# Performance work log

Measured on AMD Instinct MI355X. Metric: run time of the kernel, lower is better.

The kernel has to match this reference:

```python
import math
import jax, jax.numpy as jnp
import numpy as np

HIDDEN = 1024
HEADS = 16
HEAD_DIM = HIDDEN // HEADS  # 64
SEQ = 4096
PATCH = 4064  # num rotated (patch) tokens; last PATCH positions get RoPE
EPS = 1e-6


def setup_inputs() -> dict:
    key = jax.random.key(0)
    ks = jax.random.split(key, 8)
    return {
        "x": jax.random.normal(ks[0], (1, SEQ, HIDDEN), dtype=jnp.float32),
        "rope_cos": jax.random.uniform(ks[1], (PATCH, HEAD_DIM // 2), dtype=jnp.float32),
        "rope_sin": jax.random.uniform(ks[2], (PATCH, HEAD_DIM // 2), dtype=jnp.float32),
        "wq": jax.random.normal(ks[3], (HIDDEN, HIDDEN), dtype=jnp.float32) / math.sqrt(HIDDEN),
        "wk": jax.random.normal(ks[4], (HIDDEN, HIDDEN), dtype=jnp.float32) / math.sqrt(HIDDEN),
        "wv": jax.random.normal(ks[5], (HIDDEN, HIDDEN), dtype=jnp.float32) / math.sqrt(HIDDEN),
        "wo": jax.random.normal(ks[6], (HIDDEN, HIDDEN), dtype=jnp.float32) / math.sqrt(HIDDEN),
        "q_norm_w": jnp.ones((HEAD_DIM,), dtype=jnp.float32),
        "k_norm_w": jnp.ones((HEAD_DIM,), dtype=jnp.float32),
    }


def _rms_norm(t, w):
    # RMSNorm over the last (head_dim) axis
    return t * jax.lax.rsqrt(jnp.mean(t * t, axis=-1, keepdims=True) + EPS) * w


def _apply_rope(t, cos, sin):
    # t: [b, s, h, d]; rotate only the last PATCH positions, pairwise complex mul
    b, s, h, d = t.shape
    P = cos.shape[0]
    tail = t[:, s - P:].reshape(b, P, h, d // 2, 2)
    x0, x1 = tail[..., 0], tail[..., 1]
    c = cos[None, :, None, :]
    sn = sin[None, :, None, :]
    rot = jnp.stack([x0 * c - x1 * sn, x0 * sn + x1 * c], axis=-1).reshape(b, P, h, d)
    return jnp.concatenate([t[:, : s - P], rot], axis=1)


def reference(x, rope_cos, rope_sin, wq, wk, wv, wo, q_norm_w, k_norm_w):
    b, s, _ = x.shape
    q = (x @ wq.T).reshape(b, s, HEADS, HEAD_DIM)
    k = (x @ wk.T).reshape(b, s, HEADS, HEAD_DIM)
    v = (x @ wv.T).reshape(b, s, HEADS, HEAD_DIM)
    q = _rms_norm(q, q_norm_w)
    k = _rms_norm(k, k_norm_w)
    q = _apply_rope(q, rope_cos, rope_sin)
    k = _apply_rope(k, rope_cos, rope_sin)
    q = q / math.sqrt(HEAD_DIM)
    scores = jnp.einsum('bqhd,bkhd->bhqk', q, k)
    attn = jax.nn.softmax(scores.astype(jnp.float32), axis=-1)
    out = jnp.einsum('bhqk,bkhd->bqhd', attn, v).reshape(b, s, HIDDEN)
    return out @ wo.T
```

## Files before the change

### kernel.cpp

```cpp
#include <hip/hip_runtime.h>
#include <hip/hip_bf16.h>
#include <stdint.h>

#define HIDDEN 1024
#define HEADS 16
#define HEAD_DIM 64
#define SEQ 4096
#define PATCH 4064
#define SKIP 32

typedef __attribute__((ext_vector_type(8))) short bf16x8;
typedef __attribute__((ext_vector_type(4))) float f32x4;
typedef __attribute__((ext_vector_type(2))) float f32x2;
typedef __attribute__((ext_vector_type(16))) float f32x16;

__device__ __forceinline__ float b2f(unsigned short u){
  union{uint32_t i; float f;} c; c.i = ((uint32_t)u)<<16; return c.f;
}
__device__ __forceinline__ unsigned short f2b(float f){
  union{float f; uint32_t i;} c; c.f=f;
  uint32_t r = c.i + 0x7fffu + ((c.i>>16)&1u);
  return (unsigned short)(r>>16);
}
__device__ __forceinline__ uint32_t cvtpk(float a, float b){
  uint32_t r;
  asm("v_cvt_pk_bf16_f32 %0, %1, %2" : "=v"(r) : "v"(a), "v"(b));
  return r;
}

#define GLD16(gp, lp) __builtin_amdgcn_global_load_lds( \
    (const __attribute__((address_space(1))) void*)(gp), \
    (__attribute__((address_space(3))) void*)(lp), 16, 0, 0)

__global__ __launch_bounds__(256) void convert_all(
    const float* __restrict__ x,  const float* __restrict__ wq,
    const float* __restrict__ wk, const float* __restrict__ wv,
    const float* __restrict__ wo,
    unsigned short* __restrict__ xb,  unsigned short* __restrict__ wqb,
    unsigned short* __restrict__ wkb, unsigned short* __restrict__ wvb,
    unsigned short* __restrict__ wob)
{
  size_t u = (size_t)blockIdx.x*256 + threadIdx.x;
  size_t e = u*8;
  const float* src; unsigned short* dst; size_t off;
  if      (e < 4194304ull) { src=x;  dst=xb;  off=e;            }
  else if (e < 5242880ull) { src=wq; dst=wqb; off=e-4194304ull; }
  else if (e < 6291456ull) { src=wk; dst=wkb; off=e-5242880ull; }
  else if (e < 7340032ull) { src=wv; dst=wvb; off=e-6291456ull; }
  else                     { src=wo; dst=wob; off=e-7340032ull; }
  float4 v0 = *(const float4*)(src+off);
  float4 v1 = *(const float4*)(src+off+4);
  union { bf16x8 v; unsigned short h[8]; } o;
  o.h[0]=f2b(v0.x); o.h[1]=f2b(v0.y); o.h[2]=f2b(v0.z); o.h[3]=f2b(v0.w);
  o.h[4]=f2b(v1.x); o.h[5]=f2b(v1.y); o.h[6]=f2b(v1.z); o.h[7]=f2b(v1.w);
  *(bf16x8*)(dst+off) = o.v;
}

template<int MODE>
__global__ __launch_bounds__(256) void gemm_bt(
    const unsigned short* __restrict__ A,
    const unsigned short* __restrict__ B0,
    const unsigned short* __restrict__ B1,
    const unsigned short* __restrict__ B2,
    float* __restrict__ Cf,
    unsigned short* __restrict__ qout, unsigned short* __restrict__ kout,
    unsigned short* __restrict__ vout,
    const float* __restrict__ rc, const float* __restrict__ rs,
    const float* __restrict__ qw, const float* __restrict__ kw,
    int M, int Nper, int K)
{
  __shared__ unsigned short As[128*32];
  __shared__ unsigned short Bs[128*32];
  const int tid = threadIdx.x;
  const int w = tid>>6, l = tid&63;
  const int wm = w>>1, wn = w&1;
  const int g = l>>4, lr = l&15;
  const int bm = blockIdx.x;
  int bn = blockIdx.y;
  const int tilesPer = Nper >> 7;
  const int sel = bn / tilesPer;
  bn -= sel*tilesPer;
  const unsigned short* Bsel = (sel==0) ? B0 : ((sel==1) ? B1 : B2);

  const int off0 = w*1024 + l*16;
  const int r0 = off0>>6, c0 = (off0&63)>>1;
  const int off1 = off0 + 4096;
  const int r1 = off1>>6, c1 = (off1&63)>>1;

  const unsigned short* Ab = A    + (size_t)(bm*128)*K;
  const unsigned short* Bb = Bsel + (size_t)(bn*128)*K;

  f32x4 zero = {0.f,0.f,0.f,0.f};
  f32x4 acc[4][4];
  #pragma unroll
  for (int m=0;m<4;m++)
    #pragma unroll
    for (int n=0;n<4;n++) acc[m][n]=zero;

  for (int kt = 0; kt < K; kt += 32) {
    GLD16(Ab + (size_t)r0*K + kt + c0, (char*)As + off0);
    GLD16(Ab + (size_t)r1*K + kt + c1, (char*)As + off1);
    GLD16(Bb + (size_t)r0*K + kt + c0, (char*)Bs + off0);
    GLD16(Bb + (size_t)r1*K + kt + c1, (char*)Bs + off1);
    __syncthreads();
    bf16x8 a[4], b[4];
    #pragma unroll
    for (int m=0;m<4;m++)
      a[m] = *(const bf16x8*)&As[(wm*64 + m*16 + lr)*32 + g*8];
    #pragma unroll
    for (int n=0;n<4;n++)
      b[n] = *(const bf16x8*)&Bs[(wn*64 + n*16 + lr)*32 + g*8];
    #pragma unroll
    for (int m=0;m<4;m++)
      #pragma unroll
      for (int n=0;n<4;n++)
        acc[m][n] = __builtin_amdgcn_mfma_f32_16x16x32_bf16(a[m], b[n], acc[m][n], 0,0,0);
    __syncthreads();
  }

  if constexpr (MODE == 0) {
    #pragma unroll
    for (int m=0;m<4;m++){
      const int row = bm*128 + wm*64 + m*16 + g*4;
      #pragma unroll
      for (int n=0;n<4;n++){
        const int col = bn*128 + wn*64 + n*16 + lr;
        #pragma unroll
        for (int r=0;r<4;r++)
          Cf[(size_t)(row+r)*Nper + col] = acc[m][n][r];
      }
    }
  } else {
    if (sel <= 1) {
      const float* nw = (sel==0) ? qw : kw;
      unsigned short* dst = (sel==0) ? qout : kout;
      const float scl = (sel==0) ? 0.18033688011112042f : 1.0f;
      float wl[4];
      #pragma unroll
      for (int n=0;n<4;n++) wl[n] = nw[n*16+lr];
      const int hglob = bn*2 + wn;
      #pragma unroll
      for (int m=0;m<4;m++){
        const int rowb = bm*128 + wm*64 + m*16 + g*4;
        float rn[4];
        #pragma unroll
        for (int r=0;r<4;r++){
          float ss = 0.f;
          #pragma unroll
          for (int n=0;n<4;n++) ss += acc[m][n][r]*acc[m][n][r];
          ss += __shfl_xor(ss,1); ss += __shfl_xor(ss,2);
          ss += __shfl_xor(ss,4); ss += __shfl_xor(ss,8);
          rn[r] = rsqrtf(ss*(1.f/64.f) + 1e-6f);
        }
        #pragma unroll
        for (int r=0;r<4;r++){
          const int row = rowb + r;
          const int p = row - SKIP;
          #pragma unroll
          for (int n=0;n<4;n++){
            float v = acc[m][n][r]*rn[r]*wl[n];
            float c = 1.f, sn = 0.f;
            if (p >= 0){
              const int d2 = (n*16+lr)>>1;
              c  = rc[p*(HEAD_DIM/2) + d2];
              sn = rs[p*(HEAD_DIM/2) + d2];
            }
            const float partner = __shfl_xor(v, 1);
            const float o2 = (lr&1) ? (partner*sn + v*c) : (v*c - partner*sn);
            dst[(size_t)row*HIDDEN + hglob*64 + n*16 + lr] = f2b(o2*scl);
          }
        }
      }
    } else {
      #pragma unroll
      for (int m=0;m<4;m++){
        const int row = bm*128 + wm*64 + m*16 + g*4;
        #pragma unroll
        for (int n=0;n<4;n++){
          const int col = bn*128 + wn*64 + n*16 + lr;
          #pragma unroll
          for (int r=0;r<4;r++)
            vout[(size_t)(row+r)*HIDDEN + col] = f2b(acc[m][n][r]);
        }
      }
    }
  }
}

__global__ __launch_bounds__(256) void transpose_v(
    const unsigned short* __restrict__ v, unsigned short* __restrict__ vt)
{
  __shared__ unsigned short t[64*72];
  const int h = blockIdx.y;
  const int s0 = blockIdx.x * 64;
  const int tid = threadIdx.x;
  #pragma unroll
  for (int i=0;i<2;i++){
    const int e = tid + i*256;
    const int r = e>>3, cc = (e&7)*8;
    *(bf16x8*)&t[r*72+cc] = *(const bf16x8*)(v + (size_t)(s0+r)*HIDDEN + h*HEAD_DIM + cc);
  }
  __syncthreads();
  #pragma unroll
  for (int i=0;i<2;i++){
    const int e = tid + i*256;
    const int d = e>>3, sc = (e&7)*8;
    union { bf16x8 v8; unsigned short h8[8]; } o;
    #pragma unroll
    for (int j=0;j<8;j++){
      const int x  = sc + j;
      const int px = (x & ~12) | ((x&4)<<1) | ((x&8)>>1);
      o.h8[j] = t[px*72 + d];
    }
    *(bf16x8*)(vt + (size_t)(h*HEAD_DIM + d)*SEQ + s0 + sc) = o.v8;
  }
}

__device__ __forceinline__ void softmax_pack(f32x16 (&st)[2], f32x2 &lacc, bf16x8 (&pf)[4]){
  float pv[32];
  #pragma unroll
  for (int i=0;i<16;i++){
    pv[i]    = __builtin_amdgcn_exp2f(st[0][i]);
    pv[16+i] = __builtin_amdgcn_exp2f(st[1][i]);
  }
  #pragma unroll
  for (int i=0;i<8;i++){
    f32x2 a; a.x = pv[2*i];    a.y = pv[2*i+1];    lacc += a;
    f32x2 b; b.x = pv[16+2*i]; b.y = pv[16+2*i+1]; lacc += b;
  }
  #pragma unroll
  for (int t2=0; t2<2; t2++)
    #pragma unroll
    for (int e=0; e<2; e++){
      union { uint32_t u4[4]; bf16x8 v8; } pu;
      #pragma unroll
      for (int u=0; u<4; u++)
        pu.u4[u] = cvtpk(pv[t2*16+e*8+2*u], pv[t2*16+e*8+2*u+1]);
      pf[2*t2+e] = pu.v8;
    }
}

__global__ __launch_bounds__(256, 2) void attn_kernel(
    const unsigned short* __restrict__ q, const unsigned short* __restrict__ k,
    const unsigned short* __restrict__ vt, unsigned short* __restrict__ po,
    float* __restrict__ lbuf)
{
  __shared__ unsigned short smem[16384];
  const int fid = blockIdx.x + 16*(blockIdx.y + 16*blockIdx.z);
  const int h    = (fid&7)*2 + ((fid>>3)&1);
  const int rem  = fid>>4;
  const int q0   = (rem&15)*256;
  const int half = rem>>4;
  const int tid = threadIdx.x;
  const int w = tid>>6, l = tid&63;
  const int hi = l>>5, lo = l&31;
  const int NT = SEQ/64/2;
  const int tbase = half * NT;

  const int cA = tid, cB = tid + 256;
  const int rA = cA>>3, rB = cB>>3;
  const int colA = ((cA&7)*16) ^ ((rA&7)<<4);
  const int colB = ((cB&7)*16) ^ ((rB&7)<<4);
  const unsigned short* kA = k  + (size_t)rA*HIDDEN + h*HEAD_DIM + (colA>>1);
  const unsigned short* kB = k  + (size_t)rB*HIDDEN + h*HEAD_DIM + (colB>>1);
  const unsigned short* vA = vt + ((size_t)(h*HEAD_DIM + rA))*SEQ + (colA>>1);
  const unsigned short* vB = vt + ((size_t)(h*HEAD_DIM + rB))*SEQ + (colB>>1);

#define STAGE(b, kOffE, vOffE) do { \
    GLD16(kA + (kOffE), (char*)smem + (b)*16384 + cA*16); \
    GLD16(kB + (kOffE), (char*)smem + (b)*16384 + cB*16); \
    GLD16(vA + (vOffE), (char*)smem + (b)*16384 + 8192 + cA*16); \
    GLD16(vB + (vOffE), (char*)smem + (b)*16384 + 8192 + cB*16); \
  } while(0)

  const int swz = (lo&7)<<4;
  int colo[4];
  #pragma unroll
  for (int ks=0; ks<4; ks++) colo[ks] = ((2*ks+hi)*16) ^ swz;

  bf16x8 qf0[4], qf1[4];
  {
    const unsigned short* qp = q + (size_t)(q0 + w*64 + lo)*HIDDEN + h*HEAD_DIM;
    #pragma unroll
    for (int ks=0; ks<4; ks++){
      qf0[ks] = *(const bf16x8*)(qp + ks*16 + hi*8);
      qf1[ks] = *(const bf16x8*)(qp + 32*HIDDEN + ks*16 + hi*8);
    }
  }

  f32x16 ot0[2], ot1[2];
  #pragma unroll
  for (int m2=0;m2<2;m2++)
    #pragma unroll
    for (int i=0;i<16;i++){ ot0[m2][i] = 0.f; ot1[m2][i] = 0.f; }
  f32x2 lacc0 = {0.f,0.f}, lacc1 = {0.f,0.f};

  STAGE(0, (size_t)tbase*64*HIDDEN, (size_t)tbase*64);

  for (int t = 0; t < NT; ++t) {
    const int buf = t & 1;
    __syncthreads();
    if (t+1 < NT) {
      const size_t ta = (size_t)(tbase + t + 1);
      STAGE((t+1)&1, ta*64*HIDDEN, ta*64);
    }

    const char* Kb = (const char*)smem + buf*16384;
    const char* Vb = Kb + 8192;

    f32x16 st0[2], st1[2];
    __builtin_amdgcn_s_setprio(1);
    #pragma unroll
    for (int c=0;c<2;c++){
      #pragma unroll
      for (int i=0;i<16;i++){ st0[c][i] = 0.f; st1[c][i] = 0.f; }
      #pragma unroll
      for (int ks=0; ks<4; ks++){
        bf16x8 a = *(const bf16x8*)(Kb + (32*c+lo)*128 + colo[ks]);
        st0[c] = __builtin_amdgcn_mfma_f32_32x32x16_bf16(a, qf0[ks], st0[c], 0,0,0);
        st1[c] = __builtin_amdgcn_mfma_f32_32x32x16_bf16(a, qf1[ks], st1[c], 0,0,0);
      }
    }
    __builtin_amdgcn_s_setprio(0);

    bf16x8 pf0[4], pf1[4];
    softmax_pack(st0, lacc0, pf0);
    softmax_pack(st1, lacc1, pf1);

    __builtin_amdgcn_s_setprio(1);
    #pragma unroll
    for (int m2=0;m2<2;m2++)
      #pragma unroll
      for (int ks=0; ks<4; ks++){
        bf16x8 a = *(const bf16x8*)(Vb + (32*m2+lo)*128 + colo[ks]);
        ot0[m2] = __builtin_amdgcn_mfma_f32_32x32x16_bf16(a, pf0[ks], ot0[m2], 0,0,0);
        ot1[m2] = __builtin_amdgcn_mfma_f32_32x32x16_bf16(a, pf1[ks], ot1[m2], 0,0,0);
      }
    __builtin_amdgcn_s_setprio(0);
  }

  {
    float ls0 = lacc0.x + lacc0.y;
    ls0 += __shfl_xor(ls0, 32);
    float ls1 = lacc1.x + lacc1.y;
    ls1 += __shfl_xor(ls1, 32);
    if (hi == 0){
      lbuf[(size_t)half*HEADS*SEQ + h*SEQ + q0 + w*64 + lo]      = ls0;
      lbuf[(size_t)half*HEADS*SEQ + h*SEQ + q0 + w*64 + 32 + lo] = ls1;
    }
  }

  __syncthreads();
  #pragma unroll
  for (int m2=0;m2<2;m2++)
    #pragma unroll
    for (int f=0; f<4; f++)
      #pragma unroll
      for (int u=0; u<2; u++){
        const int d = 32*m2 + 8*f + 4*hi + 2*u;
        const uint32_t w0 = cvtpk(ot0[m2][4*f+2*u], ot0[m2][4*f+2*u+1]);
        *(uint32_t*)((char*)smem + (w*64+lo)*128 + ((d*2) ^ swz)) = w0;
        const uint32_t w1 = cvtpk(ot1[m2][4*f+2*u], ot1[m2][4*f+2*u+1]);
        *(uint32_t*)((char*)smem + (w*64+32+lo)*128 + ((d*2) ^ swz)) = w1;
      }
  __syncthreads();
  unsigned short* pout = po + (size_t)half*SEQ*HIDDEN;
  #pragma unroll
  for (int rr=0; rr<2; rr++){
    const int ql = rr*128 + (tid>>1), xh = tid&1;
    #pragma unroll
    for (int i=0;i<4;i++){
      const int cb = xh*64 + i*16;
      bf16x8 vv = *(const bf16x8*)((const char*)smem + ql*128 + (cb ^ ((ql&7)<<4)));
      *(bf16x8*)(pout + (size_t)(q0+ql)*HIDDEN + h*HEAD_DIM + (cb>>1)) = vv;
    }
  }
#undef STAGE
}

__global__ __launch_bounds__(256) void combine_halves(
    const unsigned short* __restrict__ po, const float* __restrict__ lbuf,
    unsigned short* __restrict__ at)
{
  const size_t e = ((size_t)blockIdx.x*256 + threadIdx.x)*8;
  const int qrow = (int)(e >> 10);
  const int h = (int)((e >> 6) & 15);
  const float li = 1.0f / (lbuf[h*SEQ + qrow] + lbuf[HEADS*SEQ + h*SEQ + qrow]);
  union { bf16x8 v; unsigned short s[8]; } a, b, o;
  a.v = *(const bf16x8*)(po + e);
  b.v = *(const bf16x8*)(po + (size_t)SEQ*HIDDEN + e);
  #pragma unroll
  for (int j=0;j<8;j++)
    o.s[j] = f2b((b2f(a.s[j]) + b2f(b.s[j])) * li);
  *(bf16x8*)(at + e) = o.v;
}

extern "C" void kernel_launch(void* const* d_in, const int* in_sizes, int n_in,
                              void* d_out, int out_size, void* d_ws, size_t ws_size,
                              hipStream_t stream)
{
  const float* x  = (const float*)d_in[0];
  const float* rc = (const float*)d_in[1];
  const float* rs = (const float*)d_in[2];
  const float* wq = (const float*)d_in[3];
  const float* wk = (const float*)d_in[4];
  const float* wv = (const float*)d_in[5];
  const float* wo = (const float*)d_in[6];
  const float* qw = (const float*)d_in[7];
  const float* kw = (const float*)d_in[8];
  float* out = (float*)d_out;

  char* ws = (char*)d_ws;
  const size_t MB = 1024*1024;
  unsigned short* xb  = (unsigned short*)(ws + 0);
  unsigned short* wqb = (unsigned short*)(ws + 8*MB);
  unsigned short* wkb = (unsigned short*)(ws + 10*MB);
  unsigned short* wvb = (unsigned short*)(ws + 12*MB);
  unsigned short* wob = (unsigned short*)(ws + 14*MB);
  unsigned short* qkv = (unsigned short*)(ws + 16*MB);
  unsigned short* qb = qkv;
  unsigned short* kb = qkv + (size_t)SEQ*HIDDEN;
  unsigned short* vb = qkv + (size_t)2*SEQ*HIDDEN;
  unsigned short* vt = (unsigned short*)(ws + 0);
  float*          lbuf = (float*)(ws + 8*MB);
  unsigned short* po = (unsigned short*)(ws + 32*MB);
  unsigned short* at = (unsigned short*)(ws + 40*MB);

  convert_all<<<4096, 256, 0, stream>>>(x, wq, wk, wv, wo, xb, wqb, wkb, wvb, wob);
  gemm_bt<1><<<dim3(32,24), 256, 0, stream>>>(
      xb, wqb, wkb, wvb, nullptr, qb, kb, vb, rc, rs, qw, kw,
      SEQ, HIDDEN, HIDDEN);
  transpose_v<<<dim3(64,16), 256, 0, stream>>>(vb, vt);
  attn_kernel<<<dim3(16,16,2), 256, 0, stream>>>(qb, kb, vt, po, lbuf);
  combine_halves<<<2048, 256, 0, stream>>>(po, lbuf, at);
  gemm_bt<0><<<dim3(32,8), 256, 0, stream>>>(
      at, wob, wob, wob, out, nullptr, nullptr, nullptr, nullptr, nullptr, nullptr, nullptr,
      SEQ, HIDDEN, HIDDEN);
}
```

Baseline: 181.4 us.

## Rewrite QKV projection GEMM with 256x256 tiles, double-buffered LDS and swizzle

The fused QKV projection moves to a dedicated kernel using 512-thread blocks, 256x256 output tiles, double-buffered LDS staging with an XOR swizzle, and interleaved loads and MFMAs under setprio. The aim is to hide global-load latency and LDS bank conflicts and to raise arithmetic intensity compared with the old 128x128 single-buffered loop that synchronised twice per k-step. In exchange it launches only 192 blocks, fewer than the CU count, and uses more registers, which may limit occupancy. The output GEMM is split into its own simpler kernel with unchanged behaviour.

```diff
diff --git a/kernel.cpp b/kernel.cpp
--- a/kernel.cpp
+++ b/kernel.cpp
@@ -56,18 +56,153 @@
   *(bf16x8*)(dst+off) = o.v;
 }
 
-template<int MODE>
-__global__ __launch_bounds__(256) void gemm_bt(
+__global__ __launch_bounds__(512, 2) void gemm_qkv(
     const unsigned short* __restrict__ A,
     const unsigned short* __restrict__ B0,
     const unsigned short* __restrict__ B1,
     const unsigned short* __restrict__ B2,
-    float* __restrict__ Cf,
     unsigned short* __restrict__ qout, unsigned short* __restrict__ kout,
     unsigned short* __restrict__ vout,
     const float* __restrict__ rc, const float* __restrict__ rs,
-    const float* __restrict__ qw, const float* __restrict__ kw,
-    int M, int Nper, int K)
+    const float* __restrict__ qw, const float* __restrict__ kw)
+{
+  __shared__ unsigned short smem[32768];
+  const int tid = threadIdx.x;
+  const int wid = tid>>6, l = tid&63;
+  const int wm = wid>>2, wn = wid&3;
+  const int g = l>>4, lr = l&15;
+  const int bm = blockIdx.x;
+  const int bn = blockIdx.y;
+  const int sel = bn>>2, hb = bn&3;
+  const unsigned short* Bsel = (sel==0) ? B0 : ((sel==1) ? B1 : B2);
+
+  const int strow = tid>>2;
+  const int skey = ((((tid>>2)&3) ^ ((tid>>4)&3))<<4);
+  const int scol = ((tid&3)*16) ^ skey;
+  const unsigned short* pA0 = A    + (size_t)(bm*256 + strow)*1024 + (scol>>1);
+  const unsigned short* pA1 = pA0 + (size_t)128*1024;
+  const unsigned short* pB0 = Bsel + (size_t)(hb*256 + strow)*1024 + (scol>>1);
+  const unsigned short* pB1 = pB0 + (size_t)128*1024;
+  const int dA0 = tid*16, dA1 = tid*16 + 8192;
+  const int dB0 = 16384 + tid*16, dB1 = 24576 + tid*16;
+
+#define STAGEQ(db, ktE) do { \
+    GLD16(pA0 + (ktE), (char*)smem + (db) + dA0); \
+    GLD16(pA1 + (ktE), (char*)smem + (db) + dA1); \
+    GLD16(pB0 + (ktE), (char*)smem + (db) + dB0); \
+    GLD16(pB1 + (ktE), (char*)smem + (db) + dB1); } while(0)
+
+  const int rkey = (((lr&3) ^ ((lr>>2)&3))<<4);
+  const int rcol = (g*16) ^ rkey;
+  const int aBase = (wm*128 + lr)*64 + rcol;
+  const int bBase = 16384 + (wn*64 + lr)*64 + rcol;
+
+  f32x4 acc[8][4];
+  #pragma unroll
+  for (int m=0;m<8;m++)
+    #pragma unroll
+    for (int n=0;n<4;n++) acc[m][n] = (f32x4){0.f,0.f,0.f,0.f};
+
+  STAGEQ(0, 0);
+  asm volatile("s_waitcnt vmcnt(0)" ::: "memory");
+  __builtin_amdgcn_s_barrier();
+  __builtin_amdgcn_sched_barrier(0);
+
+  for (int t = 0; t < 32; ++t) {
+    const int db  = (t&1)<<15;
+    const int ndb = db ^ 32768;
+    bf16x8 af[4], bf[4];
+    #pragma unroll
+    for (int i=0;i<4;i++) af[i] = *(const bf16x8*)((char*)smem + db + aBase + i*1024);
+    #pragma unroll
+    for (int i=0;i<4;i++) bf[i] = *(const bf16x8*)((char*)smem + db + bBase + i*1024);
+    if (t+1 < 32) STAGEQ(ndb, (t+1)*32);
+    __builtin_amdgcn_s_barrier();
+    __builtin_amdgcn_s_setprio(1);
+    #pragma unroll
+    for (int m=0;m<4;m++)
+      #pragma unroll
+      for (int n=0;n<4;n++)
+        acc[m][n] = __builtin_amdgcn_mfma_f32_16x16x32_bf16(af[m], bf[n], acc[m][n], 0,0,0);
+    __builtin_amdgcn_s_setprio(0);
+    __builtin_amdgcn_s_barrier();
+    #pragma unroll
+    for (int i=0;i<4;i++) af[i] = *(const bf16x8*)((char*)smem + db + aBase + 4096 + i*1024);
+    #pragma unroll
+    for (int i=0;i<4;i++) bf[i] = *(const bf16x8*)((char*)smem + db + bBase + i*1024);
+    asm volatile("s_waitcnt vmcnt(0)" ::: "memory");
+    __builtin_amdgcn_s_barrier();
+    __builtin_amdgcn_sched_barrier(0);
+    __builtin_amdgcn_s_setprio(1);
+    #pragma unroll
+    for (int m=0;m<4;m++)
+      #pragma unroll
+      for (int n=0;n<4;n++)
+        acc[4+m][n] = __builtin_amdgcn_mfma_f32_16x16x32_bf16(af[m], bf[n], acc[4+m][n], 0,0,0);
+    __builtin_amdgcn_s_setprio(0);
+    __builtin_amdgcn_s_barrier();
+  }
+
+  if (sel <= 1) {
+    const float* nw = (sel==0) ? qw : kw;
+    unsigned short* dst = (sel==0) ? qout : kout;
+    const float scl = (sel==0) ? 0.18033688011112042f : 1.0f;
+    float wl[4];
+    #pragma unroll
+    for (int n=0;n<4;n++) wl[n] = nw[n*16+lr];
+    const int hglob = hb*4 + wn;
+    #pragma unroll
+    for (int mf=0; mf<8; mf++){
+      const int rowb = bm*256 + wm*128 + mf*16 + g*4;
+      float rn4[4];
+      #pragma unroll
+      for (int r=0;r<4;r++){
+        float ss = 0.f;
+        #pragma unroll
+        for (int n=0;n<4;n++) ss += acc[mf][n][r]*acc[mf][n][r];
+        ss += __shfl_xor(ss,1); ss += __shfl_xor(ss,2);
+        ss += __shfl_xor(ss,4); ss += __shfl_xor(ss,8);
+        rn4[r] = rsqrtf(ss*(1.f/64.f) + 1e-6f);
+      }
+      #pragma unroll
+      for (int r=0;r<4;r++){
+        const int row = rowb + r;
+        const int p = row - SKIP;
+        #pragma unroll
+        for (int n=0;n<4;n++){
+          float v = acc[mf][n][r]*rn4[r]*wl[n];
+          float c = 1.f, sn = 0.f;
+          if (p >= 0){
+            const int d2 = (n*16+lr)>>1;
+            c  = rc[p*(HEAD_DIM/2) + d2];
+            sn = rs[p*(HEAD_DIM/2) + d2];
+          }
+          const float partner = __shfl_xor(v, 1);
+          const float o2 = (lr&1) ? (partner*sn + v*c) : (v*c - partner*sn);
+          dst[(size_t)row*HIDDEN + hglob*64 + n*16 + lr] = f2b(o2*scl);
+        }
+      }
+    }
+  } else {
+    #pragma unroll
+    for (int mf=0; mf<8; mf++){
+      const int rowb = bm*256 + wm*128 + mf*16 + g*4;
+      #pragma unroll
+      for (int n=0;n<4;n++){
+        const int col = hb*256 + wn*64 + n*16 + lr;
+        #pragma unroll
+        for (int r=0;r<4;r++)
+          vout[(size_t)(rowb+r)*HIDDEN + col] = f2b(acc[mf][n][r]);
+      }
+    }
+  }
+#undef STAGEQ
+}
+
+__global__ __launch_bounds__(256) void gemm_out(
+    const unsigned short* __restrict__ A,
+    const unsigned short* __restrict__ B,
+    float* __restrict__ Cf, int M, int N, int K)
 {
   __shared__ unsigned short As[128*32];
   __shared__ unsigned short Bs[128*32];
@@ -76,19 +211,15 @@
   const int wm = w>>1, wn = w&1;
   const int g = l>>4, lr = l&15;
   const int bm = blockIdx.x;
-  int bn = blockIdx.y;
-  const int tilesPer = Nper >> 7;
-  const int sel = bn / tilesPer;
-  bn -= sel*tilesPer;
-  const unsigned short* Bsel = (sel==0) ? B0 : ((sel==1) ? B1 : B2);
+  const int bn = blockIdx.y;
 
   const int off0 = w*1024 + l*16;
   const int r0 = off0>>6, c0 = (off0&63)>>1;
   const int off1 = off0 + 4096;
   const int r1 = off1>>6, c1 = (off1&63)>>1;
 
-  const unsigned short* Ab = A    + (size_t)(bm*128)*K;
-  const unsigned short* Bb = Bsel + (size_t)(bn*128)*K;
+  const unsigned short* Ab = A + (size_t)(bm*128)*K;
+  const unsigned short* Bb = B + (size_t)(bn*128)*K;
 
   f32x4 zero = {0.f,0.f,0.f,0.f};
   f32x4 acc[4][4];
@@ -117,72 +248,15 @@
         acc[m][n] = __builtin_amdgcn_mfma_f32_16x16x32_bf16(a[m], b[n], acc[m][n], 0,0,0);
     __syncthreads();
   }
-
-  if constexpr (MODE == 0) {
-    #pragma unroll
-    for (int m=0;m<4;m++){
-      const int row = bm*128 + wm*64 + m*16 + g*4;
-      #pragma unroll
-      for (int n=0;n<4;n++){
-        const int col = bn*128 + wn*64 + n*16 + lr;
-        #pragma unroll
-        for (int r=0;r<4;r++)
-          Cf[(size_t)(row+r)*Nper + col] = acc[m][n][r];
-      }
-    }
-  } else {
-    if (sel <= 1) {
-      const float* nw = (sel==0) ? qw : kw;
-      unsigned short* dst = (sel==0) ? qout : kout;
-      const float scl = (sel==0) ? 0.18033688011112042f : 1.0f;
-      float wl[4];
-      #pragma unroll
-      for (int n=0;n<4;n++) wl[n] = nw[n*16+lr];
-      const int hglob = bn*2 + wn;
-      #pragma unroll
-      for (int m=0;m<4;m++){
-        const int rowb = bm*128 + wm*64 + m*16 + g*4;
-        float rn[4];
-        #pragma unroll
-        for (int r=0;r<4;r++){
-          float ss = 0.f;
-          #pragma unroll
-          for (int n=0;n<4;n++) ss += acc[m][n][r]*acc[m][n][r];
-          ss += __shfl_xor(ss,1); ss += __shfl_xor(ss,2);
-          ss += __shfl_xor(ss,4); ss += __shfl_xor(ss,8);
-          rn[r] = rsqrtf(ss*(1.f/64.f) + 1e-6f);
-        }
-        #pragma unroll
-        for (int r=0;r<4;r++){
-          const int row = rowb + r;
-          const int p = row - SKIP;
-          #pragma unroll
-          for (int n=0;n<4;n++){
-            float v = acc[m][n][r]*rn[r]*wl[n];
-            float c = 1.f, sn = 0.f;
-            if (p >= 0){
-              const int d2 = (n*16+lr)>>1;
-              c  = rc[p*(HEAD_DIM/2) + d2];
-              sn = rs[p*(HEAD_DIM/2) + d2];
-            }
-            const float partner = __shfl_xor(v, 1);
-            const float o2 = (lr&1) ? (partner*sn + v*c) : (v*c - partner*sn);
-            dst[(size_t)row*HIDDEN + hglob*64 + n*16 + lr] = f2b(o2*scl);
-          }
-        }
-      }
-    } else {
-      #pragma unroll
-      for (int m=0;m<4;m++){
-        const int row = bm*128 + wm*64 + m*16 + g*4;
-        #pragma unroll
-        for (int n=0;n<4;n++){
-          const int col = bn*128 + wn*64 + n*16 + lr;
-          #pragma unroll
-          for (int r=0;r<4;r++)
-            vout[(size_t)(row+r)*HIDDEN + col] = f2b(acc[m][n][r]);
-        }
-      }
+  #pragma unroll
+  for (int m=0;m<4;m++){
+    const int row = bm*128 + wm*64 + m*16 + g*4;
+    #pragma unroll
+    for (int n=0;n<4;n++){
+      const int col = bn*128 + wn*64 + n*16 + lr;
+      #pragma unroll
+      for (int r=0;r<4;r++)
+        Cf[(size_t)(row+r)*N + col] = acc[m][n][r];
     }
   }
 }
@@ -427,13 +501,10 @@
   unsigned short* at = (unsigned short*)(ws + 40*MB);
 
   convert_all<<<4096, 256, 0, stream>>>(x, wq, wk, wv, wo, xb, wqb, wkb, wvb, wob);
-  gemm_bt<1><<<dim3(32,24), 256, 0, stream>>>(
-      xb, wqb, wkb, wvb, nullptr, qb, kb, vb, rc, rs, qw, kw,
-      SEQ, HIDDEN, HIDDEN);
+  gemm_qkv<<<dim3(16,12), 512, 0, stream>>>(
+      xb, wqb, wkb, wvb, qb, kb, vb, rc, rs, qw, kw);
   transpose_v<<<dim3(64,16), 256, 0, stream>>>(vb, vt);
   attn_kernel<<<dim3(16,16,2), 256, 0, stream>>>(qb, kb, vt, po, lbuf);
   combine_halves<<<2048, 256, 0, stream>>>(po, lbuf, at);
-  gemm_bt<0><<<dim3(32,8), 256, 0, stream>>>(
-      at, wob, wob, wob, out, nullptr, nullptr, nullptr, nullptr, nullptr, nullptr, nullptr,
-      SEQ, HIDDEN, HIDDEN);
-}
+  gemm_out<<<dim3(32,8), 256, 0, stream>>>(at, wob, out, SEQ, HIDDEN, HIDDEN);
+}
```

New measurement: 181.7 us. No clear change (+0.2%).

## Double-buffer GEMM LDS tiles and widen attention KV tiles to 128

Applied to the files above, without the earlier changes.

The projection GEMM now uses two LDS stages: the next K-slice is loaded while MFMAs run on the current one, and only one barrier per iteration remains. The attention kernel loads 128 keys per stage instead of 64 and processes them as two 64-key sub-blocks, which halves the number of barriers and stage loads. In exchange, attention LDS grows to 64KB per block, which may limit how many blocks fit per CU alongside launch_bounds(256,2).

```diff
diff --git a/kernel.cpp b/kernel.cpp
--- a/kernel.cpp
+++ b/kernel.cpp
@@ -69,8 +69,7 @@
     const float* __restrict__ qw, const float* __restrict__ kw,
     int M, int Nper, int K)
 {
-  __shared__ unsigned short As[128*32];
-  __shared__ unsigned short Bs[128*32];
+  __shared__ unsigned short smem[16384];
   const int tid = threadIdx.x;
   const int w = tid>>6, l = tid&63;
   const int wm = w>>1, wn = w&1;
@@ -90,6 +89,12 @@
   const unsigned short* Ab = A    + (size_t)(bm*128)*K;
   const unsigned short* Bb = Bsel + (size_t)(bn*128)*K;
 
+#define STG(db, kt) do { \
+    GLD16(Ab + (size_t)r0*K + (kt) + c0, (char*)smem + (db) + off0); \
+    GLD16(Ab + (size_t)r1*K + (kt) + c1, (char*)smem + (db) + off1); \
+    GLD16(Bb + (size_t)r0*K + (kt) + c0, (char*)smem + (db) + 8192 + off0); \
+    GLD16(Bb + (size_t)r1*K + (kt) + c1, (char*)smem + (db) + 8192 + off1); } while(0)
+
   f32x4 zero = {0.f,0.f,0.f,0.f};
   f32x4 acc[4][4];
   #pragma unroll
@@ -97,26 +102,26 @@
     #pragma unroll
     for (int n=0;n<4;n++) acc[m][n]=zero;
 
-  for (int kt = 0; kt < K; kt += 32) {
-    GLD16(Ab + (size_t)r0*K + kt + c0, (char*)As + off0);
-    GLD16(Ab + (size_t)r1*K + kt + c1, (char*)As + off1);
-    GLD16(Bb + (size_t)r0*K + kt + c0, (char*)Bs + off0);
-    GLD16(Bb + (size_t)r1*K + kt + c1, (char*)Bs + off1);
+  const int nkt = K >> 5;
+  STG(0, 0);
+  for (int t = 0; t < nkt; ++t) {
     __syncthreads();
+    const int db = (t&1)<<14;
+    if (t+1 < nkt) STG(db^16384, (t+1)*32);
     bf16x8 a[4], b[4];
     #pragma unroll
     for (int m=0;m<4;m++)
-      a[m] = *(const bf16x8*)&As[(wm*64 + m*16 + lr)*32 + g*8];
+      a[m] = *(const bf16x8*)((char*)smem + db + (wm*64 + m*16 + lr)*64 + g*16);
     #pragma unroll
     for (int n=0;n<4;n++)
-      b[n] = *(const bf16x8*)&Bs[(wn*64 + n*16 + lr)*32 + g*8];
+      b[n] = *(const bf16x8*)((char*)smem + db + 8192 + (wn*64 + n*16 + lr)*64 + g*16);
     #pragma unroll
     for (int m=0;m<4;m++)
       #pragma unroll
       for (int n=0;n<4;n++)
         acc[m][n] = __builtin_amdgcn_mfma_f32_16x16x32_bf16(a[m], b[n], acc[m][n], 0,0,0);
-    __syncthreads();
-  }
+  }
+#undef STG
 
   if constexpr (MODE == 0) {
     #pragma unroll
@@ -245,7 +250,7 @@
     const unsigned short* __restrict__ vt, unsigned short* __restrict__ po,
     float* __restrict__ lbuf)
 {
-  __shared__ unsigned short smem[16384];
+  __shared__ unsigned short smem[32768];
   const int fid = blockIdx.x + 16*(blockIdx.y + 16*blockIdx.z);
   const int h    = (fid&7)*2 + ((fid>>3)&1);
   const int rem  = fid>>4;
@@ -254,23 +259,35 @@
   const int tid = threadIdx.x;
   const int w = tid>>6, l = tid&63;
   const int hi = l>>5, lo = l&31;
-  const int NT = SEQ/64/2;
+  const int NT = SEQ/128/2;
   const int tbase = half * NT;
 
-  const int cA = tid, cB = tid + 256;
-  const int rA = cA>>3, rB = cB>>3;
-  const int colA = ((cA&7)*16) ^ ((rA&7)<<4);
-  const int colB = ((cB&7)*16) ^ ((rB&7)<<4);
-  const unsigned short* kA = k  + (size_t)rA*HIDDEN + h*HEAD_DIM + (colA>>1);
-  const unsigned short* kB = k  + (size_t)rB*HIDDEN + h*HEAD_DIM + (colB>>1);
-  const unsigned short* vA = vt + ((size_t)(h*HEAD_DIM + rA))*SEQ + (colA>>1);
-  const unsigned short* vB = vt + ((size_t)(h*HEAD_DIM + rB))*SEQ + (colB>>1);
+  int kcol[4], vcol[4], vrow[4];
+  #pragma unroll
+  for (int i=0;i<4;i++){
+    const int c = tid + i*256;
+    const int rk = c>>3;
+    kcol[i] = ((c&7)*16) ^ ((rk&7)<<4);
+    const int rv = c>>4;
+    vrow[i] = rv;
+    vcol[i] = (((c&7)*16) ^ ((rv&7)<<4)) + ((c>>3)&1)*128;
+  }
+  const unsigned short* kPtr[4]; const unsigned short* vPtr[4];
+  #pragma unroll
+  for (int i=0;i<4;i++){
+    kPtr[i] = k  + (size_t)((tid + i*256)>>3)*HIDDEN + h*HEAD_DIM + (kcol[i]>>1);
+    vPtr[i] = vt + ((size_t)(h*HEAD_DIM + vrow[i]))*SEQ + (vcol[i]>>1);
+  }
 
 #define STAGE(b, kOffE, vOffE) do { \
-    GLD16(kA + (kOffE), (char*)smem + (b)*16384 + cA*16); \
-    GLD16(kB + (kOffE), (char*)smem + (b)*16384 + cB*16); \
-    GLD16(vA + (vOffE), (char*)smem + (b)*16384 + 8192 + cA*16); \
-    GLD16(vB + (vOffE), (char*)smem + (b)*16384 + 8192 + cB*16); \
+    GLD16(kPtr[0] + (kOffE), (char*)smem + (b)*32768 + (tid      )*16); \
+    GLD16(kPtr[1] + (kOffE), (char*)smem + (b)*32768 + (tid+ 256 )*16); \
+    GLD16(kPtr[2] + (kOffE), (char*)smem + (b)*32768 + (tid+ 512 )*16); \
+    GLD16(kPtr[3] + (kOffE), (char*)smem + (b)*32768 + (tid+ 768 )*16); \
+    GLD16(vPtr[0] + (vOffE), (char*)smem + (b)*32768 + 16384 + (tid      )*16); \
+    GLD16(vPtr[1] + (vOffE), (char*)smem + (b)*32768 + 16384 + (tid+ 256 )*16); \
+    GLD16(vPtr[2] + (vOffE), (char*)smem + (b)*32768 + 16384 + (tid+ 512 )*16); \
+    GLD16(vPtr[3] + (vOffE), (char*)smem + (b)*32768 + 16384 + (tid+ 768 )*16); \
   } while(0)
 
   const int swz = (lo&7)<<4;
@@ -295,48 +312,51 @@
     for (int i=0;i<16;i++){ ot0[m2][i] = 0.f; ot1[m2][i] = 0.f; }
   f32x2 lacc0 = {0.f,0.f}, lacc1 = {0.f,0.f};
 
-  STAGE(0, (size_t)tbase*64*HIDDEN, (size_t)tbase*64);
+  STAGE(0, (size_t)tbase*128*HIDDEN, (size_t)tbase*128);
 
   for (int t = 0; t < NT; ++t) {
-    const int buf = t & 1;
     __syncthreads();
     if (t+1 < NT) {
       const size_t ta = (size_t)(tbase + t + 1);
-      STAGE((t+1)&1, ta*64*HIDDEN, ta*64);
-    }
-
-    const char* Kb = (const char*)smem + buf*16384;
-    const char* Vb = Kb + 8192;
-
-    f32x16 st0[2], st1[2];
-    __builtin_amdgcn_s_setprio(1);
-    #pragma unroll
-    for (int c=0;c<2;c++){
-      #pragma unroll
-      for (int i=0;i<16;i++){ st0[c][i] = 0.f; st1[c][i] = 0.f; }
-      #pragma unroll
-      for (int ks=0; ks<4; ks++){
-        bf16x8 a = *(const bf16x8*)(Kb + (32*c+lo)*128 + colo[ks]);
-        st0[c] = __builtin_amdgcn_mfma_f32_32x32x16_bf16(a, qf0[ks], st0[c], 0,0,0);
-        st1[c] = __builtin_amdgcn_mfma_f32_32x32x16_bf16(a, qf1[ks], st1[c], 0,0,0);
+      STAGE((t+1)&1, ta*128*HIDDEN, ta*128);
+    }
+    const char* Kb = (const char*)smem + (t&1)*32768;
+    const char* Vb = Kb + 16384;
+
+    #pragma unroll
+    for (int sub=0; sub<2; ++sub) {
+      const char* Ks = Kb + sub*8192;
+
+      f32x16 st0[2], st1[2];
+      __builtin_amdgcn_s_setprio(1);
+      #pragma unroll
+      for (int c=0;c<2;c++){
+        #pragma unroll
+        for (int i=0;i<16;i++){ st0[c][i] = 0.f; st1[c][i] = 0.f; }
+        #pragma unroll
+        for (int ks=0; ks<4; ks++){
+          bf16x8 a = *(const bf16x8*)(Ks + (32*c+lo)*128 + colo[ks]);
+          st0[c] = __builtin_amdgcn_mfma_f32_32x32x16_bf16(a, qf0[ks], st0[c], 0,0,0);
+          st1[c] = __builtin_amdgcn_mfma_f32_32x32x16_bf16(a, qf1[ks], st1[c], 0,0,0);
+        }
       }
-    }
-    __builtin_amdgcn_s_setprio(0);
-
-    bf16x8 pf0[4], pf1[4];
-    softmax_pack(st0, lacc0, pf0);
-    softmax_pack(st1, lacc1, pf1);
-
-    __builtin_amdgcn_s_setprio(1);
-    #pragma unroll
-    for (int m2=0;m2<2;m2++)
-      #pragma unroll
-      for (int ks=0; ks<4; ks++){
-        bf16x8 a = *(const bf16x8*)(Vb + (32*m2+lo)*128 + colo[ks]);
-        ot0[m2] = __builtin_amdgcn_mfma_f32_32x32x16_bf16(a, pf0[ks], ot0[m2], 0,0,0);
-        ot1[m2] = __builtin_amdgcn_mfma_f32_32x32x16_bf16(a, pf1[ks], ot1[m2], 0,0,0);
-      }
-    __builtin_amdgcn_s_setprio(0);
+      __builtin_amdgcn_s_setprio(0);
+
+      bf16x8 pf0[4], pf1[4];
+      softmax_pack(st0, lacc0, pf0);
+      softmax_pack(st1, lacc1, pf1);
+
+      __builtin_amdgcn_s_setprio(1);
+      #pragma unroll
+      for (int m2=0;m2<2;m2++)
+        #pragma unroll
+        for (int ks=0; ks<4; ks++){
+          bf16x8 a = *(const bf16x8*)(Vb + (32*m2+lo)*256 + sub*128 + colo[ks]);
+          ot0[m2] = __builtin_amdgcn_mfma_f32_32x32x16_bf16(a, pf0[ks], ot0[m2], 0,0,0);
+          ot1[m2] = __builtin_amdgcn_mfma_f32_32x32x16_bf16(a, pf1[ks], ot1[m2], 0,0,0);
+        }
+      __builtin_amdgcn_s_setprio(0);
+    }
   }
 
   {
```

Result: faster. 153.7 us (-15.3%).

## Split attention KV range four ways and double-buffer GEMM shared-memory tiles

Applied to the files above, without the earlier changes.

The attention kernel now splits the key/value sequence into four partitions instead of two. This doubles the grid to 1024 blocks and raises the occupancy hint to 4 blocks per CU, giving more parallel work. The extra partial outputs are placed in spare workspace and in the output buffer, and combine_halves sums four partials and four row-sum arrays. Separately, the bf16 GEMM now double-buffers its A/B tiles in shared memory, prefetching the next K-slice while computing the current one and dropping one barrier per iteration. The cost is more partial-output traffic in the combine step and possible register pressure under the higher occupancy target.

```diff
diff --git a/kernel.cpp b/kernel.cpp
--- a/kernel.cpp
+++ b/kernel.cpp
@@ -69,8 +69,7 @@
     const float* __restrict__ qw, const float* __restrict__ kw,
     int M, int Nper, int K)
 {
-  __shared__ unsigned short As[128*32];
-  __shared__ unsigned short Bs[128*32];
+  __shared__ unsigned short smem[16384];
   const int tid = threadIdx.x;
   const int w = tid>>6, l = tid&63;
   const int wm = w>>1, wn = w&1;
@@ -90,6 +89,12 @@
   const unsigned short* Ab = A    + (size_t)(bm*128)*K;
   const unsigned short* Bb = Bsel + (size_t)(bn*128)*K;
 
+#define STG(db, kt) do { \
+    GLD16(Ab + (size_t)r0*K + (kt) + c0, (char*)smem + (db) + off0); \
+    GLD16(Ab + (size_t)r1*K + (kt) + c1, (char*)smem + (db) + off1); \
+    GLD16(Bb + (size_t)r0*K + (kt) + c0, (char*)smem + (db) + 8192 + off0); \
+    GLD16(Bb + (size_t)r1*K + (kt) + c1, (char*)smem + (db) + 8192 + off1); } while(0)
+
   f32x4 zero = {0.f,0.f,0.f,0.f};
   f32x4 acc[4][4];
   #pragma unroll
@@ -97,26 +102,26 @@
     #pragma unroll
     for (int n=0;n<4;n++) acc[m][n]=zero;
 
-  for (int kt = 0; kt < K; kt += 32) {
-    GLD16(Ab + (size_t)r0*K + kt + c0, (char*)As + off0);
-    GLD16(Ab + (size_t)r1*K + kt + c1, (char*)As + off1);
-    GLD16(Bb + (size_t)r0*K + kt + c0, (char*)Bs + off0);
-    GLD16(Bb + (size_t)r1*K + kt + c1, (char*)Bs + off1);
+  const int nkt = K >> 5;
+  STG(0, 0);
+  for (int t = 0; t < nkt; ++t) {
     __syncthreads();
+    const int db = (t&1)<<14;
+    if (t+1 < nkt) STG(db^16384, (t+1)*32);
     bf16x8 a[4], b[4];
     #pragma unroll
     for (int m=0;m<4;m++)
-      a[m] = *(const bf16x8*)&As[(wm*64 + m*16 + lr)*32 + g*8];
+      a[m] = *(const bf16x8*)((char*)smem + db + (wm*64 + m*16 + lr)*64 + g*16);
     #pragma unroll
     for (int n=0;n<4;n++)
-      b[n] = *(const bf16x8*)&Bs[(wn*64 + n*16 + lr)*32 + g*8];
+      b[n] = *(const bf16x8*)((char*)smem + db + 8192 + (wn*64 + n*16 + lr)*64 + g*16);
     #pragma unroll
     for (int m=0;m<4;m++)
       #pragma unroll
       for (int n=0;n<4;n++)
         acc[m][n] = __builtin_amdgcn_mfma_f32_16x16x32_bf16(a[m], b[n], acc[m][n], 0,0,0);
-    __syncthreads();
-  }
+  }
+#undef STG
 
   if constexpr (MODE == 0) {
     #pragma unroll
@@ -240,9 +245,11 @@
     }
 }
 
-__global__ __launch_bounds__(256, 2) void attn_kernel(
+__global__ __launch_bounds__(256, 4) void attn_kernel(
     const unsigned short* __restrict__ q, const unsigned short* __restrict__ k,
-    const unsigned short* __restrict__ vt, unsigned short* __restrict__ po,
+    const unsigned short* __restrict__ vt,
+    unsigned short* __restrict__ po0, unsigned short* __restrict__ po1,
+    unsigned short* __restrict__ po2, unsigned short* __restrict__ po3,
     float* __restrict__ lbuf)
 {
   __shared__ unsigned short smem[16384];
@@ -254,7 +261,7 @@
   const int tid = threadIdx.x;
   const int w = tid>>6, l = tid&63;
   const int hi = l>>5, lo = l&31;
-  const int NT = SEQ/64/2;
+  const int NT = SEQ/64/4;
   const int tbase = half * NT;
 
   const int cA = tid, cB = tid + 256;
@@ -298,14 +305,12 @@
   STAGE(0, (size_t)tbase*64*HIDDEN, (size_t)tbase*64);
 
   for (int t = 0; t < NT; ++t) {
-    const int buf = t & 1;
     __syncthreads();
     if (t+1 < NT) {
       const size_t ta = (size_t)(tbase + t + 1);
       STAGE((t+1)&1, ta*64*HIDDEN, ta*64);
     }
-
-    const char* Kb = (const char*)smem + buf*16384;
+    const char* Kb = (const char*)smem + (t&1)*16384;
     const char* Vb = Kb + 8192;
 
     f32x16 st0[2], st1[2];
@@ -364,7 +369,7 @@
         *(uint32_t*)((char*)smem + (w*64+32+lo)*128 + ((d*2) ^ swz)) = w1;
       }
   __syncthreads();
-  unsigned short* pout = po + (size_t)half*SEQ*HIDDEN;
+  unsigned short* pout = (half==0) ? po0 : (half==1) ? po1 : (half==2) ? po2 : po3;
   #pragma unroll
   for (int rr=0; rr<2; rr++){
     const int ql = rr*128 + (tid>>1), xh = tid&1;
@@ -379,19 +384,24 @@
 }
 
 __global__ __launch_bounds__(256) void combine_halves(
-    const unsigned short* __restrict__ po, const float* __restrict__ lbuf,
-    unsigned short* __restrict__ at)
+    const unsigned short* __restrict__ po0, const unsigned short* __restrict__ po1,
+    const unsigned short* __restrict__ po2, const unsigned short* __restrict__ po3,
+    const float* __restrict__ lbuf, unsigned short* __restrict__ at)
 {
   const size_t e = ((size_t)blockIdx.x*256 + threadIdx.x)*8;
   const int qrow = (int)(e >> 10);
   const int h = (int)((e >> 6) & 15);
-  const float li = 1.0f / (lbuf[h*SEQ + qrow] + lbuf[HEADS*SEQ + h*SEQ + qrow]);
-  union { bf16x8 v; unsigned short s[8]; } a, b, o;
-  a.v = *(const bf16x8*)(po + e);
-  b.v = *(const bf16x8*)(po + (size_t)SEQ*HIDDEN + e);
+  const int li0 = h*SEQ + qrow;
+  const float li = 1.0f / (lbuf[li0] + lbuf[HEADS*SEQ + li0]
+                         + lbuf[2*HEADS*SEQ + li0] + lbuf[3*HEADS*SEQ + li0]);
+  union { bf16x8 v; unsigned short s[8]; } a, b, c, d, o;
+  a.v = *(const bf16x8*)(po0 + e);
+  b.v = *(const bf16x8*)(po1 + e);
+  c.v = *(const bf16x8*)(po2 + e);
+  d.v = *(const bf16x8*)(po3 + e);
   #pragma unroll
   for (int j=0;j<8;j++)
-    o.s[j] = f2b((b2f(a.s[j]) + b2f(b.s[j])) * li);
+    o.s[j] = f2b((b2f(a.s[j]) + b2f(b.s[j]) + b2f(c.s[j]) + b2f(d.s[j])) * li);
   *(bf16x8*)(at + e) = o.v;
 }
 
@@ -423,16 +433,19 @@
   unsigned short* vb = qkv + (size_t)2*SEQ*HIDDEN;
   unsigned short* vt = (unsigned short*)(ws + 0);
   float*          lbuf = (float*)(ws + 8*MB);
-  unsigned short* po = (unsigned short*)(ws + 32*MB);
-  unsigned short* at = (unsigned short*)(ws + 40*MB);
+  unsigned short* po0 = (unsigned short*)(ws + 32*MB);
+  unsigned short* po1 = (unsigned short*)(ws + 40*MB);
+  unsigned short* po2 = (unsigned short*)out;
+  unsigned short* po3 = (unsigned short*)out + (size_t)SEQ*HIDDEN;
+  unsigned short* at  = po1;
 
   convert_all<<<4096, 256, 0, stream>>>(x, wq, wk, wv, wo, xb, wqb, wkb, wvb, wob);
   gemm_bt<1><<<dim3(32,24), 256, 0, stream>>>(
       xb, wqb, wkb, wvb, nullptr, qb, kb, vb, rc, rs, qw, kw,
       SEQ, HIDDEN, HIDDEN);
   transpose_v<<<dim3(64,16), 256, 0, stream>>>(vb, vt);
-  attn_kernel<<<dim3(16,16,2), 256, 0, stream>>>(qb, kb, vt, po, lbuf);
-  combine_halves<<<2048, 256, 0, stream>>>(po, lbuf, at);
+  attn_kernel<<<dim3(16,16,4), 256, 0, stream>>>(qb, kb, vt, po0, po1, po2, po3, lbuf);
+  combine_halves<<<2048, 256, 0, stream>>>(po0, po1, po2, po3, lbuf, at);
   gemm_bt<0><<<dim3(32,8), 256, 0, stream>>>(
       at, wob, wob, wob, out, nullptr, nullptr, nullptr, nullptr, nullptr, nullptr, nullptr,
       SEQ, HIDDEN, HIDDEN);
```

New measurement: 619.4 us. 3.41x slower.
